# Performance work log

Measured on AMD Instinct MI355X. Metric: run time of the kernel, lower is better.

The kernel has to match this reference:

```python
import jax, jax.numpy as jnp
import numpy as np

N_NODES = 100_000
N_EDGES = 1_200_000
N_GRAPHS = 256
HIT_IN, VAR_IN = 5, 19
H = 64            # hit_embed_dim (h_feat of ResGCN)
D = 128           # transformer hidden = hit + var embed
N_GNN, N_ENC, HEADS, NCLS = 6, 6, 8, 2
EPS = 1e-7        # GENConv message eps


def _ln(x, g, b, eps=1e-5):
    m = jnp.mean(x, -1, keepdims=True)
    v = jnp.mean((x - m) ** 2, -1, keepdims=True)
    return (x - m) * jax.lax.rsqrt(v + eps) * g + b


def _forward(floats, edge_index, batch):
    (x, var_data, enc_W, enc_b, ln_g, ln_b, t_param, mlp1_W, mlp1_b,
     mlpn_g, mlpn_b, mlp2_W, mlp2_b, v1_W, v1_b, v2_W, v2_b, v3_W, v3_b,
     qkv_W, qkv_b, out_W, out_b, ln1_g, ln1_b, ff1_W, ff1_b, ff2_W, ff2_b,
     ln2_g, ln2_b, head_W, head_b) = floats
    src, dst = edge_index[0], edge_index[1]
    N = x.shape[0]
    h = x @ enc_W + enc_b                                   # [N, H]
    for i in range(N_GNN):
        # DeepGCNLayer block='res+': norm -> relu -> conv, then residual add
        z = jax.nn.relu(_ln(h, ln_g[i], ln_b[i]))
        # GENConv aggr='softmax': per-channel segment softmax over incoming edges
        msg = jax.nn.relu(z[src]) + EPS                     # [E, H]
        s = msg * t_param[i]
        m = jax.lax.stop_gradient(jax.ops.segment_max(s, dst, num_segments=N))
        m = jnp.where(jnp.isfinite(m), m, 0.0)
        e = jnp.exp(s - m[dst])
        den = jax.ops.segment_sum(e, dst, num_segments=N)
        alpha = e / jnp.maximum(den, 1e-16)[dst]
        agg = jax.ops.segment_sum(msg * alpha, dst, num_segments=N)
        # GENConv: out = mlp(agg + x_dst); MLP = Lin(H,2H)->LN->ReLU->Lin(2H,H)
        u = z + agg
        u = jax.nn.relu(_ln(u @ mlp1_W[i] + mlp1_b[i], mlpn_g[i], mlpn_b[i]))
        u = u @ mlp2_W[i] + mlp2_b[i]
        h = h + u
    pooled = jax.ops.segment_sum(h, batch, num_segments=N_GRAPHS)  # [B, H]
    # VariableEmbed MLP 19->16->32->64
    v = jax.nn.relu(var_data @ v1_W + v1_b)
    v = jax.nn.relu(v @ v2_W + v2_b)
    v = v @ v3_W + v3_b
    # reshape(-1,1,D) -> seq_len = num_graphs, batch = 1 (post-norm encoder)
    t = jnp.concatenate([pooled, v], -1)                    # [B, D]
    S = t.shape[0]
    dh = D // HEADS
    for i in range(N_ENC):
        qkv = t @ qkv_W[i] + qkv_b[i]
        q, k, vv = jnp.split(qkv, 3, axis=-1)
        q = q.reshape(S, HEADS, dh).transpose(1, 0, 2)
        k = k.reshape(S, HEADS, dh).transpose(1, 0, 2)
        vv = vv.reshape(S, HEADS, dh).transpose(1, 0, 2)
        att = jax.nn.softmax(jnp.einsum('hqd,hkd->hqk', q, k) / jnp.sqrt(jnp.float32(dh)), axis=-1)
        o = jnp.einsum('hqk,hkd->hqd', att, vv).transpose(1, 0, 2).reshape(S, D)
        o = o @ out_W[i] + out_b[i]
        t = _ln(t + o, ln1_g[i], ln1_b[i])
        f = jax.nn.gelu(t @ ff1_W[i] + ff1_b[i], approximate=False)
        f = f @ ff2_W[i] + ff2_b[i]
        t = _ln(t + f, ln2_g[i], ln2_b[i])
    return t @ head_W + head_b                              # [B, NCLS]


FLOAT_KEYS = ['x', 'var_data', 'enc_W', 'enc_b', 'ln_g', 'ln_b', 't_param',
              'mlp1_W', 'mlp1_b', 'mlpn_g', 'mlpn_b', 'mlp2_W', 'mlp2_b',
              'v1_W', 'v1_b', 'v2_W', 'v2_b', 'v3_W', 'v3_b',
              'qkv_W', 'qkv_b', 'out_W', 'out_b', 'ln1_g', 'ln1_b',
              'ff1_W', 'ff1_b', 'ff2_W', 'ff2_b', 'ln2_g', 'ln2_b',
              'head_W', 'head_b']


def setup_inputs() -> dict:
    key = jax.random.key(0)
    ks = iter(jax.random.split(key, 64))
    def nrm(shape, s=0.05):
        return jax.random.normal(next(ks), shape, jnp.float32) * s
    return {
        'x': jax.random.normal(next(ks), (N_NODES, HIT_IN), jnp.float32),
        'edge_index': jax.random.randint(next(ks), (2, N_EDGES), 0, N_NODES),
        'batch': jnp.sort(jax.random.randint(next(ks), (N_NODES,), 0, N_GRAPHS)),
        'var_data': jax.random.normal(next(ks), (N_GRAPHS, VAR_IN), jnp.float32),
        'enc_W': nrm((HIT_IN, H)), 'enc_b': jnp.zeros((H,)),
        'ln_g': jnp.ones((N_GNN, H)), 'ln_b': jnp.zeros((N_GNN, H)),
        't_param': jnp.ones((N_GNN,)),
        'mlp1_W': nrm((N_GNN, H, 2 * H)), 'mlp1_b': jnp.zeros((N_GNN, 2 * H)),
        'mlpn_g': jnp.ones((N_GNN, 2 * H)), 'mlpn_b': jnp.zeros((N_GNN, 2 * H)),
        'mlp2_W': nrm((N_GNN, 2 * H, H)), 'mlp2_b': jnp.zeros((N_GNN, H)),
        'v1_W': nrm((VAR_IN, 16)), 'v1_b': jnp.zeros((16,)),
        'v2_W': nrm((16, 32)), 'v2_b': jnp.zeros((32,)),
        'v3_W': nrm((32, 64)), 'v3_b': jnp.zeros((64,)),
        'qkv_W': nrm((N_ENC, D, 3 * D)), 'qkv_b': jnp.zeros((N_ENC, 3 * D)),
        'out_W': nrm((N_ENC, D, D)), 'out_b': jnp.zeros((N_ENC, D)),
        'ln1_g': jnp.ones((N_ENC, D)), 'ln1_b': jnp.zeros((N_ENC, D)),
        'ff1_W': nrm((N_ENC, D, D)), 'ff1_b': jnp.zeros((N_ENC, D)),
        'ff2_W': nrm((N_ENC, D, D)), 'ff2_b': jnp.zeros((N_ENC, D)),
        'ln2_g': jnp.ones((N_ENC, D)), 'ln2_b': jnp.zeros((N_ENC, D)),
        'head_W': nrm((D, NCLS)), 'head_b': jnp.zeros((NCLS,)),
    }


def reference(x, edge_index, batch, var_data, enc_W, enc_b, ln_g, ln_b, t_param,
              mlp1_W, mlp1_b, mlpn_g, mlpn_b, mlp2_W, mlp2_b,
              v1_W, v1_b, v2_W, v2_b, v3_W, v3_b,
              qkv_W, qkv_b, out_W, out_b, ln1_g, ln1_b,
              ff1_W, ff1_b, ff2_W, ff2_b, ln2_g, ln2_b, head_W, head_b):
    floats = (x, var_data, enc_W, enc_b, ln_g, ln_b, t_param, mlp1_W, mlp1_b,
              mlpn_g, mlpn_b, mlp2_W, mlp2_b, v1_W, v1_b, v2_W, v2_b, v3_W, v3_b,
              qkv_W, qkv_b, out_W, out_b, ln1_g, ln1_b, ff1_W, ff1_b, ff2_W, ff2_b,
              ln2_g, ln2_b, head_W, head_b)
    return _forward(floats, edge_index, batch)
```

## Files before the change

### kernel.cpp

```cpp
#include <hip/hip_runtime.h>
#include <hip/hip_bf16.h>
#include <math.h>

#define NODES 100000
#define EDGES 1200000
#define NG 256

typedef unsigned short u16;
typedef unsigned int   u32;
typedef __attribute__((ext_vector_type(8))) short bf16x8;
typedef __attribute__((ext_vector_type(4))) float f32x4;

__device__ __forceinline__ u16 f2bf(float f){
  u32 u = __float_as_uint(f);
  u32 r = (u + 0x7FFFu + ((u >> 16) & 1u)) >> 16;
  return (u16)r;
}
__device__ __forceinline__ float bf2f(u16 b){ return __uint_as_float(((u32)b) << 16); }
__device__ __forceinline__ float bfL(u32 v){ return __uint_as_float(v << 16); }
__device__ __forceinline__ float bfH(u32 v){ return __uint_as_float(v & 0xFFFF0000u); }

__device__ __forceinline__ float wsum64(float v){
  v += __shfl_xor(v, 32); v += __shfl_xor(v, 16); v += __shfl_xor(v, 8);
  v += __shfl_xor(v, 4);  v += __shfl_xor(v, 2);  v += __shfl_xor(v, 1);
  return v;
}
__device__ __forceinline__ float wmax64(float v){
  v = fmaxf(v, __shfl_xor(v, 32)); v = fmaxf(v, __shfl_xor(v, 16));
  v = fmaxf(v, __shfl_xor(v, 8));  v = fmaxf(v, __shfl_xor(v, 4));
  v = fmaxf(v, __shfl_xor(v, 2));  v = fmaxf(v, __shfl_xor(v, 1));
  return v;
}
__device__ __forceinline__ float bsum256(float v, float* red){
  v = wsum64(v);
  if ((threadIdx.x & 63) == 0) red[threadIdx.x >> 6] = v;
  __syncthreads();
  float r = red[0] + red[1] + red[2] + red[3];
  __syncthreads();
  return r;
}

__global__ void k_zero2(int* counts, float* pooled){
  int i = blockIdx.x*256 + threadIdx.x;
  if (i < NODES) counts[i] = 0;
  if (i < NG*64) pooled[i] = 0.f;
}

__global__ void k_wprep(const float* __restrict__ m1W, const float* __restrict__ m2W,
                        u16* __restrict__ w1t_g, u16* __restrict__ w2t_g){
  int idx = blockIdx.x*256 + threadIdx.x;
  if (idx < 49152){
    int L = idx >> 13, r = idx & 8191, j = r >> 6, k = r & 63;
    w1t_g[idx] = f2bf(m1W[(L << 13) + k*128 + j]);
  } else if (idx < 98304){
    int t = idx - 49152;
    int L = t >> 13, r = t & 8191, j = r >> 7, k = r & 127;
    w2t_g[t] = f2bf(m2W[(L << 13) + k*64 + j]);
  }
}

__global__ void k_hist(const int* __restrict__ dst, int* __restrict__ counts){
  int e = blockIdx.x*256 + threadIdx.x;
  if (e < EDGES) atomicAdd(&counts[dst[e]], 1);
}

__global__ void k_scan1(const int* __restrict__ counts, int* __restrict__ rowptr, int* __restrict__ bsums){
  __shared__ int sd[256];
  int tid = threadIdx.x;
  int base = blockIdx.x*2048 + tid*8;
  int v[8]; int s = 0;
  #pragma unroll
  for (int i = 0; i < 8; i++){
    int idx = base + i;
    int c = (idx < NODES) ? counts[idx] : 0;
    v[i] = s; s += c;
  }
  sd[tid] = s;
  __syncthreads();
  for (int off = 1; off < 256; off <<= 1){
    int t = 0;
    if (tid >= off) t = sd[tid - off];
    __syncthreads();
    if (tid >= off) sd[tid] += t;
    __syncthreads();
  }
  int excl = (tid > 0) ? sd[tid-1] : 0;
  #pragma unroll
  for (int i = 0; i < 8; i++){
    int idx = base + i;
    if (idx < NODES) rowptr[idx] = v[i] + excl;
  }
  if (tid == 255) bsums[blockIdx.x] = sd[255];
}

__global__ void k_scan2(const int* __restrict__ bsums, int* __restrict__ boffs, int nb){
  int tid = threadIdx.x;
  int acc = 0;
  for (int j = 0; j < nb; j++){
    int b = bsums[j];
    if (j < tid) acc += b;
  }
  if (tid < nb) boffs[tid] = acc;
}

__global__ void k_scan3(int* __restrict__ rowptr, int* __restrict__ cursor, const int* __restrict__ boffs){
  int i = blockIdx.x*256 + threadIdx.x;
  if (i < NODES){
    int r = rowptr[i] + boffs[i >> 11];
    rowptr[i] = r; cursor[i] = r;
  }
  if (i == 0) rowptr[NODES] = EDGES;
}

__global__ void k_scatter(const int* __restrict__ src, const int* __restrict__ dst,
                          int* __restrict__ cursor, int* __restrict__ esrc){
  int e = blockIdx.x*256 + threadIdx.x;
  if (e < EDGES){
    int d = dst[e];
    int p = atomicAdd(&cursor[d], 1);
    esrc[p] = src[e];
  }
}

__global__ __launch_bounds__(256) void k_enc(const float* __restrict__ x,
    const float* __restrict__ encW, const float* __restrict__ encb,
    const float* __restrict__ lg, const float* __restrict__ lb,
    float* __restrict__ h, u16* __restrict__ z){
  __shared__ float we[320], wb[64], sg[64], sb[64];
  int tid = threadIdx.x;
  for (int i = tid; i < 320; i += 256) we[i] = encW[i];
  if (tid < 64){ wb[tid] = encb[tid]; sg[tid] = lg[tid]; sb[tid] = lb[tid]; }
  __syncthreads();
  int n = blockIdx.x*256 + tid;
  if (n >= NODES) return;
  float xv[5];
  #pragma unroll
  for (int k = 0; k < 5; k++) xv[k] = x[n*5 + k];
  float a[64];
  #pragma unroll
  for (int c = 0; c < 64; c++){
    float t = wb[c];
    #pragma unroll
    for (int k = 0; k < 5; k++) t += xv[k]*we[k*64 + c];
    a[c] = t;
  }
  float mean = 0.f;
  #pragma unroll
  for (int c = 0; c < 64; c++) mean += a[c];
  mean *= (1.f/64.f);
  float var = 0.f;
  #pragma unroll
  for (int c = 0; c < 64; c++){ float d = a[c]-mean; var += d*d; }
  var *= (1.f/64.f);
  float rstd = rsqrtf(var + 1e-5f);
  size_t rb = (size_t)n*64;
  #pragma unroll
  for (int c = 0; c < 64; c += 4){
    *(float4*)&h[rb + c] = make_float4(a[c], a[c+1], a[c+2], a[c+3]);
    ushort4 zv;
    zv.x = f2bf(fmaxf((a[c  ]-mean)*rstd*sg[c  ]+sb[c  ], 0.f));
    zv.y = f2bf(fmaxf((a[c+1]-mean)*rstd*sg[c+1]+sb[c+1], 0.f));
    zv.z = f2bf(fmaxf((a[c+2]-mean)*rstd*sg[c+2]+sb[c+2], 0.f));
    zv.w = f2bf(fmaxf((a[c+3]-mean)*rstd*sg[c+3]+sb[c+3], 0.f));
    *(ushort4*)&z[rb + c] = zv;
  }
}

__global__ __launch_bounds__(256) void k_agg(const u32* __restrict__ z32, u32* __restrict__ uo,
    const int* __restrict__ rowptr, const int* __restrict__ esrc,
    const float* __restrict__ tparam, int li){
  int lane = threadIdx.x & 63;
  int half = lane >> 5;
  int c2 = lane & 31;
  int n = blockIdx.x*8 + (threadIdx.x >> 6)*2 + half;
  if (n >= NODES) return;
  float tp = tparam[li];
  int beg = rowptr[n], end = rowptr[n+1];
  u32 zp = z32[(size_t)n*32 + c2];
  float zn0 = bfL(zp), zn1 = bfH(zp);
  float den0 = 0.f, num0 = 0.f, den1 = 0.f, num1 = 0.f;
  int e = beg;
  for (; e + 7 < end; e += 8){
    int si[8];
    #pragma unroll
    for (int r = 0; r < 8; r++) si[r] = esrc[e + r];
    u32 vv[8];
    #pragma unroll
    for (int r = 0; r < 8; r++) vv[r] = z32[(size_t)si[r]*32 + c2];
    #pragma unroll
    for (int r = 0; r < 8; r++){
      float m0 = bfL(vv[r]) + 1e-7f, m1 = bfH(vv[r]) + 1e-7f;
      float e0 = __expf(m0*tp), e1 = __expf(m1*tp);
      den0 += e0; num0 += m0*e0;
      den1 += e1; num1 += m1*e1;
    }
  }
  for (; e + 3 < end; e += 4){
    int si[4];
    #pragma unroll
    for (int r = 0; r < 4; r++) si[r] = esrc[e + r];
    u32 vv[4];
    #pragma unroll
    for (int r = 0; r < 4; r++) vv[r] = z32[(size_t)si[r]*32 + c2];
    #pragma unroll
    for (int r = 0; r < 4; r++){
      float m0 = bfL(vv[r]) + 1e-7f, m1 = bfH(vv[r]) + 1e-7f;
      float e0 = __expf(m0*tp), e1 = __expf(m1*tp);
      den0 += e0; num0 += m0*e0;
      den1 += e1; num1 += m1*e1;
    }
  }
  for (; e < end; ++e){
    u32 v = z32[(size_t)esrc[e]*32 + c2];
    float m0 = bfL(v) + 1e-7f, m1 = bfH(v) + 1e-7f;
    float e0 = __expf(m0*tp), e1 = __expf(m1*tp);
    den0 += e0; num0 += m0*e0;
    den1 += e1; num1 += m1*e1;
  }
  float u0 = zn0 + num0 / fmaxf(den0, 1e-16f);
  float u1 = zn1 + num1 / fmaxf(den1, 1e-16f);
  uo[(size_t)n*32 + c2] = (u32)f2bf(u0) | ((u32)f2bf(u1) << 16);
}

__global__ __launch_bounds__(256) void k_mlpm(
    const u16* __restrict__ u, float* __restrict__ h, u16* __restrict__ znext,
    float* __restrict__ pooled, const int* __restrict__ batch,
    const u16* __restrict__ w1t_g, const u16* __restrict__ w2t_g,
    const float* __restrict__ B1, const float* __restrict__ G1, const float* __restrict__ Q1,
    const float* __restrict__ B2, const float* __restrict__ GN, const float* __restrict__ BN,
    int last){
  __shared__ u16 w1t[128*88];
  __shared__ u16 w2t[64*152];
  __shared__ float cb1[128], cg1[128], cq1[128];
  __shared__ float cb2[64], cgn[64], cbn[64];
  int tid = threadIdx.x;
  const uint4* w1g = (const uint4*)w1t_g;
  const uint4* w2g = (const uint4*)w2t_g;
  for (int i = tid; i < 1024; i += 256){
    { int j = i >> 3, c = i & 7;  *(uint4*)&w1t[j*88  + c*8] = w1g[i]; }
    { int j = i >> 4, c = i & 15; *(uint4*)&w2t[j*152 + c*8] = w2g[i]; }
  }
  if (tid < 128){ cb1[tid] = B1[tid]; cg1[tid] = G1[tid]; cq1[tid] = Q1[tid]; }
  if (tid < 64){
    cb2[tid] = B2[tid];
    cgn[tid] = last ? 0.f : GN[tid];
    cbn[tid] = last ? 0.f : BN[tid];
  }
  __syncthreads();

  int w = tid >> 6, l = tid & 63, l15 = l & 15, g = l >> 4;
  int nd = w*16 + l15;
  int base0 = blockIdx.x*128;
  int hi = g >> 1;
  int s0l = ((g & 1) << 5) + l15;
  int s1l = s0l + 16;
  f32x4 zero4 = {0.f, 0.f, 0.f, 0.f};
  bf16x8 bz8 = {0,0,0,0,0,0,0,0};

  bf16x8 buA[2], buB[2];
  #pragma unroll
  for (int it = 0; it < 2; it++){
    int node = base0 + it*64 + nd;
    bool ok = node < NODES;
    buA[it] = ok ? *(const bf16x8*)&u[(size_t)node*64 +      g*8] : bz8;
    buB[it] = ok ? *(const bf16x8*)&u[(size_t)node*64 + 32 + g*8] : bz8;
  }

  #pragma unroll
  for (int it = 0; it < 2; it++){
    int node = base0 + it*64 + nd;
    bool ok = node < NODES;
    f32x4 c1[8];
    #pragma unroll
    for (int mt = 0; mt < 8; mt++) c1[mt] = zero4;
    #pragma unroll
    for (int mt = 0; mt < 8; mt++){
      bf16x8 aw0 = *(const bf16x8*)&w1t[(mt*16 + l15)*88 +      g*8];
      c1[mt] = __builtin_amdgcn_mfma_f32_16x16x32_bf16(aw0, buA[it], c1[mt], 0, 0, 0);
      bf16x8 aw1 = *(const bf16x8*)&w1t[(mt*16 + l15)*88 + 32 + g*8];
      c1[mt] = __builtin_amdgcn_mfma_f32_16x16x32_bf16(aw1, buB[it], c1[mt], 0, 0, 0);
    }
    float sum = 0.f, sq = 0.f;
    #pragma unroll
    for (int mt = 0; mt < 8; mt++){
      #pragma unroll
      for (int r = 0; r < 4; r++){
        float v = c1[mt][r] + cb1[mt*16 + g*4 + r];
        c1[mt][r] = v;
        sum += v; sq += v*v;
      }
    }
    sum += __shfl_xor(sum, 16); sum += __shfl_xor(sum, 32);
    sq  += __shfl_xor(sq, 16);  sq  += __shfl_xor(sq, 32);
    float mean = sum*(1.f/128.f);
    float var  = sq*(1.f/128.f) - mean*mean;
    float rstd = rsqrtf(fmaxf(var, 0.f) + 1e-5f);
    u32 pk0[8], pk1[8];
    #pragma unroll
    for (int mt = 0; mt < 8; mt++){
      int ch = mt*16 + g*4;
      float a0 = fmaxf((c1[mt][0]-mean)*rstd*cg1[ch  ] + cq1[ch  ], 0.f);
      float a1 = fmaxf((c1[mt][1]-mean)*rstd*cg1[ch+1] + cq1[ch+1], 0.f);
      float a2 = fmaxf((c1[mt][2]-mean)*rstd*cg1[ch+2] + cq1[ch+2], 0.f);
      float a3 = fmaxf((c1[mt][3]-mean)*rstd*cg1[ch+3] + cq1[ch+3], 0.f);
      pk0[mt] = (u32)f2bf(a0) | ((u32)f2bf(a1) << 16);
      pk1[mt] = (u32)f2bf(a2) | ((u32)f2bf(a3) << 16);
    }
    f32x4 c2[4];
    #pragma unroll
    for (int mt = 0; mt < 4; mt++) c2[mt] = zero4;
    #pragma unroll
    for (int ks = 0; ks < 4; ks++){
      u32 x0 = pk0[2*ks], x1 = pk0[2*ks+1];
      u32 y0 = pk1[2*ks], y1 = pk1[2*ks+1];
      u32 a0 = (u32)__shfl((int)x0, s0l), a1 = (u32)__shfl((int)x1, s0l);
      u32 b0 = (u32)__shfl((int)y0, s0l), b1 = (u32)__shfl((int)y1, s0l);
      u32 c0 = (u32)__shfl((int)x0, s1l), c1v = (u32)__shfl((int)x1, s1l);
      u32 d0 = (u32)__shfl((int)y0, s1l), d1 = (u32)__shfl((int)y1, s1l);
      union { u32 q[4]; bf16x8 v; } bb;
      bb.q[0] = hi ? a1 : a0;
      bb.q[1] = hi ? b1 : b0;
      bb.q[2] = hi ? c1v : c0;
      bb.q[3] = hi ? d1 : d0;
      #pragma unroll
      for (int mt = 0; mt < 4; mt++){
        bf16x8 aw = *(const bf16x8*)&w2t[(mt*16 + l15)*152 + ks*32 + g*8];
        c2[mt] = __builtin_amdgcn_mfma_f32_16x16x32_bf16(aw, bb.v, c2[mt], 0, 0, 0);
      }
    }
    if (ok){
      float out[16];
      size_t hb = (size_t)node*64;
      #pragma unroll
      for (int mt = 0; mt < 4; mt++){
        int ch = mt*16 + g*4;
        float4 hv = *(const float4*)&h[hb + ch];
        out[mt*4  ] = c2[mt][0] + cb2[ch  ] + hv.x;
        out[mt*4+1] = c2[mt][1] + cb2[ch+1] + hv.y;
        out[mt*4+2] = c2[mt][2] + cb2[ch+2] + hv.z;
        out[mt*4+3] = c2[mt][3] + cb2[ch+3] + hv.w;
      }
      if (!last){
        #pragma unroll
        for (int mt = 0; mt < 4; mt++){
          int ch = mt*16 + g*4;
          *(float4*)&h[hb + ch] = make_float4(out[mt*4], out[mt*4+1], out[mt*4+2], out[mt*4+3]);
        }
        float s2 = 0.f, q2 = 0.f;
        #pragma unroll
        for (int c = 0; c < 16; c++){ s2 += out[c]; q2 += out[c]*out[c]; }
        s2 += __shfl_xor(s2, 16); s2 += __shfl_xor(s2, 32);
        q2 += __shfl_xor(q2, 16); q2 += __shfl_xor(q2, 32);
        float m2 = s2*(1.f/64.f);
        float v2 = q2*(1.f/64.f) - m2*m2;
        float rs2 = rsqrtf(fmaxf(v2, 0.f) + 1e-5f);
        #pragma unroll
        for (int mt = 0; mt < 4; mt++){
          int ch = mt*16 + g*4;
          u16 z0 = f2bf(fmaxf((out[mt*4  ]-m2)*rs2*cgn[ch  ] + cbn[ch  ], 0.f));
          u16 z1 = f2bf(fmaxf((out[mt*4+1]-m2)*rs2*cgn[ch+1] + cbn[ch+1], 0.f));
          u16 z2 = f2bf(fmaxf((out[mt*4+2]-m2)*rs2*cgn[ch+2] + cbn[ch+2], 0.f));
          u16 z3 = f2bf(fmaxf((out[mt*4+3]-m2)*rs2*cgn[ch+3] + cbn[ch+3], 0.f));
          uint2 pk; pk.x = (u32)z0 | ((u32)z1 << 16); pk.y = (u32)z2 | ((u32)z3 << 16);
          *(uint2*)&znext[hb + ch] = pk;
        }
      } else {
        int gb = batch[node];
        #pragma unroll
        for (int c = 0; c < 16; c++){
          int ch = (c >> 2)*16 + g*4 + (c & 3);
          atomicAdd(&pooled[gb*64 + ch], out[c]);
        }
      }
    }
  }
}

__global__ __launch_bounds__(128) void k_pool2(
    const float* __restrict__ pooled, const float* __restrict__ var_data,
    const float* __restrict__ v1W, const float* __restrict__ v1b,
    const float* __restrict__ v2W, const float* __restrict__ v2b,
    const float* __restrict__ v3W, const float* __restrict__ v3b,
    float* __restrict__ t, float* __restrict__ qkvout,
    const float* __restrict__ qW, const float* __restrict__ qb){
  __shared__ float vin[19], l1[16], l2[32], tr[128];
  int c = threadIdx.x, s = blockIdx.x;
  if (c < 19) vin[c] = var_data[s*19 + c];
  __syncthreads();
  if (c < 16){
    float a = v1b[c];
    for (int k = 0; k < 19; k++) a += vin[k]*v1W[k*16 + c];
    l1[c] = fmaxf(a, 0.f);
  }
  __syncthreads();
  if (c < 32){
    float a = v2b[c];
    for (int k = 0; k < 16; k++) a += l1[k]*v2W[k*32 + c];
    l2[c] = fmaxf(a, 0.f);
  }
  __syncthreads();
  float tv;
  if (c < 64) tv = pooled[s*64 + c];
  else {
    float a = v3b[c-64];
    for (int k = 0; k < 32; k++) a += l2[k]*v3W[k*64 + (c-64)];
    tv = a;
  }
  tr[c] = tv; t[s*128 + c] = tv;
  __syncthreads();
  #pragma unroll 1
  for (int r = 0; r < 3; r++){
    int col = r*128 + c;
    float a = qb[col];
    #pragma unroll 4
    for (int k = 0; k < 128; k++) a += tr[k]*qW[k*384 + col];
    qkvout[s*384 + col] = a;
  }
}

__global__ __launch_bounds__(256) void k_attrow(
    const float* __restrict__ qkv, float* __restrict__ t, float* __restrict__ qkvout,
    const float* __restrict__ outW, const float* __restrict__ outb,
    const float* __restrict__ l1g, const float* __restrict__ l1b,
    const float* __restrict__ f1W, const float* __restrict__ f1b,
    const float* __restrict__ f2W, const float* __restrict__ f2b,
    const float* __restrict__ l2g, const float* __restrict__ l2b,
    const float* __restrict__ qW, const float* __restrict__ qb,
    const float* __restrict__ hW, const float* __restrict__ hb2,
    float* __restrict__ dout, int last){
  __shared__ float kv[8448];
  __shared__ float sc[8*260];
  __shared__ float qrow[128], orow[128], strow[128], s1row[128], sfrow[128], t2row[128];
  __shared__ float red[4];
  int tid = threadIdx.x, s = blockIdx.x;
  if (tid < 128){ qrow[tid] = qkv[(size_t)s*384 + tid]; strow[tid] = t[(size_t)s*128 + tid]; }
  for (int tile = 0; tile < 4; tile++){
    __syncthreads();
    for (int i = tid; i < 8192; i += 256){
      int r = i >> 7, c = i & 127;
      kv[r*132 + c] = qkv[(size_t)(tile*64 + r)*384 + 128 + c];
    }
    __syncthreads();
    int j = tid >> 2, sub = tid & 3;
    float d0 = 0.f, d1 = 0.f;
    #pragma unroll
    for (int d = 0; d < 16; d++){
      d0 += qrow[sub*16 + d]     * kv[j*132 + sub*16 + d];
      d1 += qrow[(sub+4)*16 + d] * kv[j*132 + (sub+4)*16 + d];
    }
    sc[sub*260     + tile*64 + j] = d0*0.25f;
    sc[(sub+4)*260 + tile*64 + j] = d1*0.25f;
  }
  __syncthreads();
  {
    int wid = tid >> 6, lane = tid & 63;
    #pragma unroll
    for (int hh = 0; hh < 2; hh++){
      int hh2 = wid*2 + hh;
      float a0 = sc[hh2*260 + lane], a1 = sc[hh2*260 + 64 + lane];
      float a2 = sc[hh2*260 + 128 + lane], a3 = sc[hh2*260 + 192 + lane];
      float m = wmax64(fmaxf(fmaxf(a0,a1), fmaxf(a2,a3)));
      float e0 = __expf(a0-m), e1 = __expf(a1-m), e2 = __expf(a2-m), e3 = __expf(a3-m);
      float sum = wsum64((e0+e1)+(e2+e3));
      float inv = 1.f/sum;
      sc[hh2*260 + lane] = e0*inv; sc[hh2*260 + 64 + lane] = e1*inv;
      sc[hh2*260 + 128 + lane] = e2*inv; sc[hh2*260 + 192 + lane] = e3*inv;
    }
  }
  float o = 0.f;
  int hme = (tid & 127) >> 4;
  for (int tile = 0; tile < 4; tile++){
    __syncthreads();
    for (int i = tid; i < 8192; i += 256){
      int r = i >> 7, c = i & 127;
      kv[r*132 + c] = qkv[(size_t)(tile*64 + r)*384 + 256 + c];
    }
    __syncthreads();
    if (tid < 128){
      #pragma unroll 4
      for (int j = 0; j < 64; j++)
        o += sc[hme*260 + tile*64 + j] * kv[j*132 + tid];
    }
  }
  if (tid < 128) orow[tid] = o;
  float acc = (tid < 128) ? outb[tid] : 0.f;
  for (int kt = 0; kt < 4; kt++){
    __syncthreads();
    for (int i = tid; i < 4096; i += 256) kv[i] = outW[(size_t)kt*4096 + i];
    __syncthreads();
    if (tid < 128){
      #pragma unroll 8
      for (int kk = 0; kk < 32; kk++) acc += orow[kt*32 + kk]*kv[kk*128 + tid];
    }
  }
  if (tid < 128) acc += strow[tid];
  float mean = bsum256((tid < 128) ? acc : 0.f, red)*(1.f/128.f);
  float d0v = (tid < 128) ? (acc - mean) : 0.f;
  float var = bsum256(d0v*d0v, red)*(1.f/128.f);
  float t1 = 0.f;
  if (tid < 128){
    t1 = d0v*rsqrtf(var + 1e-5f)*l1g[tid] + l1b[tid];
    s1row[tid] = t1;
  }
  float f = (tid < 128) ? f1b[tid] : 0.f;
  for (int kt = 0; kt < 4; kt++){
    __syncthreads();
    for (int i = tid; i < 4096; i += 256) kv[i] = f1W[(size_t)kt*4096 + i];
    __syncthreads();
    if (tid < 128){
      #pragma unroll 8
      for (int kk = 0; kk < 32; kk++) f += s1row[kt*32 + kk]*kv[kk*128 + tid];
    }
  }
  if (tid < 128){
    f = 0.5f*f*(1.f + erff(f*0.70710678118654752f));
    sfrow[tid] = f;
  }
  float g = (tid < 128) ? f2b[tid] : 0.f;
  for (int kt = 0; kt < 4; kt++){
    __syncthreads();
    for (int i = tid; i < 4096; i += 256) kv[i] = f2W[(size_t)kt*4096 + i];
    __syncthreads();
    if (tid < 128){
      #pragma unroll 8
      for (int kk = 0; kk < 32; kk++) g += sfrow[kt*32 + kk]*kv[kk*128 + tid];
    }
  }
  if (tid < 128) g += t1;
  float mean2 = bsum256((tid < 128) ? g : 0.f, red)*(1.f/128.f);
  float d2v = (tid < 128) ? (g - mean2) : 0.f;
  float var2 = bsum256(d2v*d2v, red)*(1.f/128.f);
  if (tid < 128){
    float t2 = d2v*rsqrtf(var2 + 1e-5f)*l2g[tid] + l2b[tid];
    t[(size_t)s*128 + tid] = t2;
    t2row[tid] = t2;
  }
  __syncthreads();
  if (!last){
    float a0 = qb[tid];
    float a1 = (tid < 128) ? qb[256 + tid] : 0.f;
    for (int kt = 0; kt < 8; kt++){
      __syncthreads();
      for (int i = tid; i < 6144; i += 256) kv[i] = qW[(size_t)kt*6144 + i];
      __syncthreads();
      #pragma unroll 4
      for (int kk = 0; kk < 16; kk++){
        float tv = t2row[kt*16 + kk];
        a0 += tv*kv[kk*384 + tid];
        if (tid < 128) a1 += tv*kv[kk*384 + 256 + tid];
      }
    }
    qkvout[(size_t)s*384 + tid] = a0;
    if (tid < 128) qkvout[(size_t)s*384 + 256 + tid] = a1;
  } else {
    if (tid < 2){
      float a = hb2[tid];
      for (int k = 0; k < 128; k++) a += t2row[k]*hW[k*2 + tid];
      dout[s*2 + tid] = a;
    }
  }
}

extern "C" void kernel_launch(void* const* d_in, const int* in_sizes, int n_in,
                              void* d_out, int out_size, void* d_ws, size_t ws_size,
                              hipStream_t stream){
  const float* x       = (const float*)d_in[0];
  const int*   ei      = (const int*)  d_in[1];
  const int*   batch   = (const int*)  d_in[2];
  const float* var_d   = (const float*)d_in[3];
  const float* encW    = (const float*)d_in[4];
  const float* encb    = (const float*)d_in[5];
  const float* ln_g    = (const float*)d_in[6];
  const float* ln_b    = (const float*)d_in[7];
  const float* tparam  = (const float*)d_in[8];
  const float* m1W     = (const float*)d_in[9];
  const float* m1b     = (const float*)d_in[10];
  const float* mng     = (const float*)d_in[11];
  const float* mnb     = (const float*)d_in[12];
  const float* m2W     = (const float*)d_in[13];
  const float* m2b     = (const float*)d_in[14];
  const float* v1W     = (const float*)d_in[15];
  const float* v1b     = (const float*)d_in[16];
  const float* v2W     = (const float*)d_in[17];
  const float* v2b     = (const float*)d_in[18];
  const float* v3W     = (const float*)d_in[19];
  const float* v3b     = (const float*)d_in[20];
  const float* qkvW    = (const float*)d_in[21];
  const float* qkvB    = (const float*)d_in[22];
  const float* outW    = (const float*)d_in[23];
  const float* outb    = (const float*)d_in[24];
  const float* l1g     = (const float*)d_in[25];
  const float* l1b     = (const float*)d_in[26];
  const float* f1W     = (const float*)d_in[27];
  const float* f1b     = (const float*)d_in[28];
  const float* f2W     = (const float*)d_in[29];
  const float* f2b     = (const float*)d_in[30];
  const float* l2g     = (const float*)d_in[31];
  const float* l2b     = (const float*)d_in[32];
  const float* headW   = (const float*)d_in[33];
  const float* headB   = (const float*)d_in[34];
  float* dout = (float*)d_out;

  char* wsb = (char*)d_ws;
  size_t off = 0;
  auto nxt = [&](size_t bytes)->void*{
    void* p = wsb + off;
    off += (bytes + 255) & ~(size_t)255;
    return p;
  };
  float* h      = (float*)nxt((size_t)NODES*64*4);
  u16*   z      = (u16*)  nxt((size_t)NODES*64*2);
  u16*   u      = (u16*)  nxt((size_t)NODES*64*2);
  int*   rowptr = (int*)  nxt((size_t)(NODES+1)*4);
  int*   cursor = (int*)  nxt((size_t)NODES*4);
  int*   counts = (int*)  nxt((size_t)NODES*4);
  int*   bsums  = (int*)  nxt(64*4);
  int*   boffs  = (int*)  nxt(64*4);
  int*   esrc   = (int*)  nxt((size_t)EDGES*4);
  float* pooled = (float*)nxt((size_t)NG*64*4);
  float* tbuf   = (float*)nxt((size_t)NG*128*4);
  float* qkv0   = (float*)nxt((size_t)NG*384*4);
  float* qkv1   = (float*)nxt((size_t)NG*384*4);
  u16*   w1tg   = (u16*)  nxt((size_t)49152*2);
  u16*   w2tg   = (u16*)  nxt((size_t)49152*2);
  float* qkvb[2] = { qkv0, qkv1 };

  const int* srcp = ei;
  const int* dstp = ei + EDGES;

  k_zero2  <<<391, 256, 0, stream>>>(counts, pooled);
  k_wprep  <<<384, 256, 0, stream>>>(m1W, m2W, w1tg, w2tg);
  k_hist   <<<4688, 256, 0, stream>>>(dstp, counts);
  k_scan1  <<<49, 256, 0, stream>>>(counts, rowptr, bsums);
  k_scan2  <<<1, 64, 0, stream>>>(bsums, boffs, 49);
  k_scan3  <<<391, 256, 0, stream>>>(rowptr, cursor, boffs);
  k_scatter<<<4688, 256, 0, stream>>>(srcp, dstp, cursor, esrc);
  k_enc    <<<391, 256, 0, stream>>>(x, encW, encb, ln_g, ln_b, h, z);

  for (int i = 0; i < 6; i++){
    int last = (i == 5);
    k_agg <<<12500, 256, 0, stream>>>((const u32*)z, (u32*)u, rowptr, esrc, tparam, i);
    k_mlpm<<<782, 256, 0, stream>>>(u, h, z, pooled, batch,
        w1tg + i*8192, w2tg + i*8192,
        m1b + i*128, mng + i*128, mnb + i*128,
        m2b + i*64,
        ln_g + (last ? 0 : (i+1)*64), ln_b + (last ? 0 : (i+1)*64), last);
  }

  k_pool2<<<NG, 128, 0, stream>>>(pooled, var_d, v1W, v1b, v2W, v2b, v3W, v3b,
                                  tbuf, qkv0, qkvW, qkvB);

  for (int i = 0; i < 6; i++){
    int last = (i == 5);
    k_attrow<<<NG, 256, 0, stream>>>(qkvb[i & 1], tbuf, qkvb[(i + 1) & 1],
        outW + i*16384, outb + i*128, l1g + i*128, l1b + i*128,
        f1W + i*16384, f1b + i*128, f2W + i*16384, f2b + i*128,
        l2g + i*128, l2b + i*128,
        qkvW + (size_t)(last ? 0 : (i+1))*49152, qkvB + (last ? 0 : (i+1))*384,
        headW, headB, dout, last);
  }
}
```

Baseline: 1.501 ms.

## Store residual and QKV in bf16, widen agg lanes, merge init kernels

Stores the residual stream h and the transformer QKV buffers in bf16 instead of fp32, which halves their memory traffic. Changes the aggregation kernel so each lane handles four channels with uint2 loads, giving 16 lanes per node and half as many blocks. Merges the zeroing and weight-prep kernels into one launch. Accumulating the residual in bf16 across six layers adds rounding error and risks accuracy.

Result: faster. 1.444 ms (-3.8%).

```diff
diff --git a/kernel.cpp b/kernel.cpp
--- a/kernel.cpp
+++ b/kernel.cpp
@@ -19,6 +19,7 @@
 __device__ __forceinline__ float bf2f(u16 b){ return __uint_as_float(((u32)b) << 16); }
 __device__ __forceinline__ float bfL(u32 v){ return __uint_as_float(v << 16); }
 __device__ __forceinline__ float bfH(u32 v){ return __uint_as_float(v & 0xFFFF0000u); }
+__device__ __forceinline__ u32 pk2(float a, float b){ return (u32)f2bf(a) | ((u32)f2bf(b) << 16); }
 
 __device__ __forceinline__ float wsum64(float v){
   v += __shfl_xor(v, 32); v += __shfl_xor(v, 16); v += __shfl_xor(v, 8);
@@ -40,19 +41,17 @@
   return r;
 }
 
-__global__ void k_zero2(int* counts, float* pooled){
-  int i = blockIdx.x*256 + threadIdx.x;
-  if (i < NODES) counts[i] = 0;
-  if (i < NG*64) pooled[i] = 0.f;
-}
-
-__global__ void k_wprep(const float* __restrict__ m1W, const float* __restrict__ m2W,
-                        u16* __restrict__ w1t_g, u16* __restrict__ w2t_g){
+__global__ void k_init(int* counts, float* pooled,
+                       const float* __restrict__ m1W, const float* __restrict__ m2W,
+                       u16* __restrict__ w1t_g, u16* __restrict__ w2t_g){
   int idx = blockIdx.x*256 + threadIdx.x;
+  if (idx < NODES) counts[idx] = 0;
+  if (idx < NG*64) pooled[idx] = 0.f;
   if (idx < 49152){
     int L = idx >> 13, r = idx & 8191, j = r >> 6, k = r & 63;
     w1t_g[idx] = f2bf(m1W[(L << 13) + k*128 + j]);
-  } else if (idx < 98304){
+  }
+  if (idx < 98304 && idx >= 49152){
     int t = idx - 49152;
     int L = t >> 13, r = t & 8191, j = r >> 7, k = r & 127;
     w2t_g[t] = f2bf(m2W[(L << 13) + k*64 + j]);
@@ -125,7 +124,7 @@
 __global__ __launch_bounds__(256) void k_enc(const float* __restrict__ x,
     const float* __restrict__ encW, const float* __restrict__ encb,
     const float* __restrict__ lg, const float* __restrict__ lb,
-    float* __restrict__ h, u16* __restrict__ z){
+    u16* __restrict__ hbf, u16* __restrict__ z){
   __shared__ float we[320], wb[64], sg[64], sb[64];
   int tid = threadIdx.x;
   for (int i = tid; i < 320; i += 256) we[i] = encW[i];
@@ -156,13 +155,15 @@
   size_t rb = (size_t)n*64;
   #pragma unroll
   for (int c = 0; c < 64; c += 4){
-    *(float4*)&h[rb + c] = make_float4(a[c], a[c+1], a[c+2], a[c+3]);
-    ushort4 zv;
-    zv.x = f2bf(fmaxf((a[c  ]-mean)*rstd*sg[c  ]+sb[c  ], 0.f));
-    zv.y = f2bf(fmaxf((a[c+1]-mean)*rstd*sg[c+1]+sb[c+1], 0.f));
-    zv.z = f2bf(fmaxf((a[c+2]-mean)*rstd*sg[c+2]+sb[c+2], 0.f));
-    zv.w = f2bf(fmaxf((a[c+3]-mean)*rstd*sg[c+3]+sb[c+3], 0.f));
-    *(ushort4*)&z[rb + c] = zv;
+    uint2 hv;
+    hv.x = pk2(a[c], a[c+1]); hv.y = pk2(a[c+2], a[c+3]);
+    *(uint2*)&hbf[rb + c] = hv;
+    uint2 zv;
+    zv.x = pk2(fmaxf((a[c  ]-mean)*rstd*sg[c  ]+sb[c  ], 0.f),
+               fmaxf((a[c+1]-mean)*rstd*sg[c+1]+sb[c+1], 0.f));
+    zv.y = pk2(fmaxf((a[c+2]-mean)*rstd*sg[c+2]+sb[c+2], 0.f),
+               fmaxf((a[c+3]-mean)*rstd*sg[c+3]+sb[c+3], 0.f));
+    *(uint2*)&z[rb + c] = zv;
   }
 }
 
@@ -170,60 +171,71 @@
     const int* __restrict__ rowptr, const int* __restrict__ esrc,
     const float* __restrict__ tparam, int li){
   int lane = threadIdx.x & 63;
-  int half = lane >> 5;
-  int c2 = lane & 31;
-  int n = blockIdx.x*8 + (threadIdx.x >> 6)*2 + half;
+  int q  = lane >> 4;
+  int cl = lane & 15;
+  int n = blockIdx.x*16 + (threadIdx.x >> 6)*4 + q;
   if (n >= NODES) return;
   float tp = tparam[li];
   int beg = rowptr[n], end = rowptr[n+1];
-  u32 zp = z32[(size_t)n*32 + c2];
-  float zn0 = bfL(zp), zn1 = bfH(zp);
-  float den0 = 0.f, num0 = 0.f, den1 = 0.f, num1 = 0.f;
+  const uint2* zq = (const uint2*)z32;
+  uint2 zp = zq[(size_t)n*16 + cl];
+  float zn0 = bfL(zp.x), zn1 = bfH(zp.x), zn2 = bfL(zp.y), zn3 = bfH(zp.y);
+  float den0=0.f,num0=0.f,den1=0.f,num1=0.f,den2=0.f,num2=0.f,den3=0.f,num3=0.f;
   int e = beg;
   for (; e + 7 < end; e += 8){
     int si[8];
     #pragma unroll
     for (int r = 0; r < 8; r++) si[r] = esrc[e + r];
-    u32 vv[8];
-    #pragma unroll
-    for (int r = 0; r < 8; r++) vv[r] = z32[(size_t)si[r]*32 + c2];
+    uint2 vv[8];
+    #pragma unroll
+    for (int r = 0; r < 8; r++) vv[r] = zq[(size_t)si[r]*16 + cl];
     #pragma unroll
     for (int r = 0; r < 8; r++){
-      float m0 = bfL(vv[r]) + 1e-7f, m1 = bfH(vv[r]) + 1e-7f;
-      float e0 = __expf(m0*tp), e1 = __expf(m1*tp);
+      float m0 = bfL(vv[r].x) + 1e-7f, m1 = bfH(vv[r].x) + 1e-7f;
+      float m2 = bfL(vv[r].y) + 1e-7f, m3 = bfH(vv[r].y) + 1e-7f;
+      float e0 = __expf(m0*tp), e1 = __expf(m1*tp), e2 = __expf(m2*tp), e3 = __expf(m3*tp);
       den0 += e0; num0 += m0*e0;
       den1 += e1; num1 += m1*e1;
+      den2 += e2; num2 += m2*e2;
+      den3 += e3; num3 += m3*e3;
     }
   }
   for (; e + 3 < end; e += 4){
     int si[4];
     #pragma unroll
     for (int r = 0; r < 4; r++) si[r] = esrc[e + r];
-    u32 vv[4];
-    #pragma unroll
-    for (int r = 0; r < 4; r++) vv[r] = z32[(size_t)si[r]*32 + c2];
+    uint2 vv[4];
+    #pragma unroll
+    for (int r = 0; r < 4; r++) vv[r] = zq[(size_t)si[r]*16 + cl];
     #pragma unroll
     for (int r = 0; r < 4; r++){
-      float m0 = bfL(vv[r]) + 1e-7f, m1 = bfH(vv[r]) + 1e-7f;
-      float e0 = __expf(m0*tp), e1 = __expf(m1*tp);
+      float m0 = bfL(vv[r].x) + 1e-7f, m1 = bfH(vv[r].x) + 1e-7f;
+      float m2 = bfL(vv[r].y) + 1e-7f, m3 = bfH(vv[r].y) + 1e-7f;
+      float e0 = __expf(m0*tp), e1 = __expf(m1*tp), e2 = __expf(m2*tp), e3 = __expf(m3*tp);
       den0 += e0; num0 += m0*e0;
       den1 += e1; num1 += m1*e1;
+      den2 += e2; num2 += m2*e2;
+      den3 += e3; num3 += m3*e3;
     }
   }
   for (; e < end; ++e){
-    u32 v = z32[(size_t)esrc[e]*32 + c2];
-    float m0 = bfL(v) + 1e-7f, m1 = bfH(v) + 1e-7f;
-    float e0 = __expf(m0*tp), e1 = __expf(m1*tp);
+    uint2 v = zq[(size_t)esrc[e]*16 + cl];
+    float m0 = bfL(v.x) + 1e-7f, m1 = bfH(v.x) + 1e-7f;
+    float m2 = bfL(v.y) + 1e-7f, m3 = bfH(v.y) + 1e-7f;
+    float e0 = __expf(m0*tp), e1 = __expf(m1*tp), e2 = __expf(m2*tp), e3 = __expf(m3*tp);
     den0 += e0; num0 += m0*e0;
     den1 += e1; num1 += m1*e1;
-  }
-  float u0 = zn0 + num0 / fmaxf(den0, 1e-16f);
-  float u1 = zn1 + num1 / fmaxf(den1, 1e-16f);
-  uo[(size_t)n*32 + c2] = (u32)f2bf(u0) | ((u32)f2bf(u1) << 16);
+    den2 += e2; num2 += m2*e2;
+    den3 += e3; num3 += m3*e3;
+  }
+  uint2 o;
+  o.x = pk2(zn0 + num0 / fmaxf(den0, 1e-16f), zn1 + num1 / fmaxf(den1, 1e-16f));
+  o.y = pk2(zn2 + num2 / fmaxf(den2, 1e-16f), zn3 + num3 / fmaxf(den3, 1e-16f));
+  ((uint2*)uo)[(size_t)n*16 + cl] = o;
 }
 
 __global__ __launch_bounds__(256) void k_mlpm(
-    const u16* __restrict__ u, float* __restrict__ h, u16* __restrict__ znext,
+    const u16* __restrict__ u, u16* __restrict__ hbf, u16* __restrict__ znext,
     float* __restrict__ pooled, const int* __restrict__ batch,
     const u16* __restrict__ w1t_g, const u16* __restrict__ w2t_g,
     const float* __restrict__ B1, const float* __restrict__ G1, const float* __restrict__ Q1,
@@ -303,8 +315,8 @@
       float a1 = fmaxf((c1[mt][1]-mean)*rstd*cg1[ch+1] + cq1[ch+1], 0.f);
       float a2 = fmaxf((c1[mt][2]-mean)*rstd*cg1[ch+2] + cq1[ch+2], 0.f);
       float a3 = fmaxf((c1[mt][3]-mean)*rstd*cg1[ch+3] + cq1[ch+3], 0.f);
-      pk0[mt] = (u32)f2bf(a0) | ((u32)f2bf(a1) << 16);
-      pk1[mt] = (u32)f2bf(a2) | ((u32)f2bf(a3) << 16);
+      pk0[mt] = pk2(a0, a1);
+      pk1[mt] = pk2(a2, a3);
     }
     f32x4 c2[4];
     #pragma unroll
@@ -334,17 +346,20 @@
       #pragma unroll
       for (int mt = 0; mt < 4; mt++){
         int ch = mt*16 + g*4;
-        float4 hv = *(const float4*)&h[hb + ch];
-        out[mt*4  ] = c2[mt][0] + cb2[ch  ] + hv.x;
-        out[mt*4+1] = c2[mt][1] + cb2[ch+1] + hv.y;
-        out[mt*4+2] = c2[mt][2] + cb2[ch+2] + hv.z;
-        out[mt*4+3] = c2[mt][3] + cb2[ch+3] + hv.w;
+        uint2 hv = *(const uint2*)&hbf[hb + ch];
+        out[mt*4  ] = c2[mt][0] + cb2[ch  ] + bfL(hv.x);
+        out[mt*4+1] = c2[mt][1] + cb2[ch+1] + bfH(hv.x);
+        out[mt*4+2] = c2[mt][2] + cb2[ch+2] + bfL(hv.y);
+        out[mt*4+3] = c2[mt][3] + cb2[ch+3] + bfH(hv.y);
       }
       if (!last){
         #pragma unroll
         for (int mt = 0; mt < 4; mt++){
           int ch = mt*16 + g*4;
-          *(float4*)&h[hb + ch] = make_float4(out[mt*4], out[mt*4+1], out[mt*4+2], out[mt*4+3]);
+          uint2 hv;
+          hv.x = pk2(out[mt*4  ], out[mt*4+1]);
+          hv.y = pk2(out[mt*4+2], out[mt*4+3]);
+          *(uint2*)&hbf[hb + ch] = hv;
         }
         float s2 = 0.f, q2 = 0.f;
         #pragma unroll
@@ -357,11 +372,11 @@
         #pragma unroll
         for (int mt = 0; mt < 4; mt++){
           int ch = mt*16 + g*4;
-          u16 z0 = f2bf(fmaxf((out[mt*4  ]-m2)*rs2*cgn[ch  ] + cbn[ch  ], 0.f));
-          u16 z1 = f2bf(fmaxf((out[mt*4+1]-m2)*rs2*cgn[ch+1] + cbn[ch+1], 0.f));
-          u16 z2 = f2bf(fmaxf((out[mt*4+2]-m2)*rs2*cgn[ch+2] + cbn[ch+2], 0.f));
-          u16 z3 = f2bf(fmaxf((out[mt*4+3]-m2)*rs2*cgn[ch+3] + cbn[ch+3], 0.f));
-          uint2 pk; pk.x = (u32)z0 | ((u32)z1 << 16); pk.y = (u32)z2 | ((u32)z3 << 16);
+          uint2 pk;
+          pk.x = pk2(fmaxf((out[mt*4  ]-m2)*rs2*cgn[ch  ] + cbn[ch  ], 0.f),
+                     fmaxf((out[mt*4+1]-m2)*rs2*cgn[ch+1] + cbn[ch+1], 0.f));
+          pk.y = pk2(fmaxf((out[mt*4+2]-m2)*rs2*cgn[ch+2] + cbn[ch+2], 0.f),
+                     fmaxf((out[mt*4+3]-m2)*rs2*cgn[ch+3] + cbn[ch+3], 0.f));
           *(uint2*)&znext[hb + ch] = pk;
         }
       } else {
@@ -381,7 +396,7 @@
     const float* __restrict__ v1W, const float* __restrict__ v1b,
     const float* __restrict__ v2W, const float* __restrict__ v2b,
     const float* __restrict__ v3W, const float* __restrict__ v3b,
-    float* __restrict__ t, float* __restrict__ qkvout,
+    float* __restrict__ t, u16* __restrict__ qkvout,
     const float* __restrict__ qW, const float* __restrict__ qb){
   __shared__ float vin[19], l1[16], l2[32], tr[128];
   int c = threadIdx.x, s = blockIdx.x;
@@ -414,12 +429,12 @@
     float a = qb[col];
     #pragma unroll 4
     for (int k = 0; k < 128; k++) a += tr[k]*qW[k*384 + col];
-    qkvout[s*384 + col] = a;
+    qkvout[s*384 + col] = f2bf(a);
   }
 }
 
 __global__ __launch_bounds__(256) void k_attrow(
-    const float* __restrict__ qkv, float* __restrict__ t, float* __restrict__ qkvout,
+    const u16* __restrict__ qkv, float* __restrict__ t, u16* __restrict__ qkvout,
     const float* __restrict__ outW, const float* __restrict__ outb,
     const float* __restrict__ l1g, const float* __restrict__ l1b,
     const float* __restrict__ f1W, const float* __restrict__ f1b,
@@ -433,12 +448,15 @@
   __shared__ float qrow[128], orow[128], strow[128], s1row[128], sfrow[128], t2row[128];
   __shared__ float red[4];
   int tid = threadIdx.x, s = blockIdx.x;
-  if (tid < 128){ qrow[tid] = qkv[(size_t)s*384 + tid]; strow[tid] = t[(size_t)s*128 + tid]; }
+  const u32* qkv32 = (const u32*)qkv;
+  if (tid < 128){ qrow[tid] = bf2f(qkv[(size_t)s*384 + tid]); strow[tid] = t[(size_t)s*128 + tid]; }
   for (int tile = 0; tile < 4; tile++){
     __syncthreads();
-    for (int i = tid; i < 8192; i += 256){
-      int r = i >> 7, c = i & 127;
-      kv[r*132 + c] = qkv[(size_t)(tile*64 + r)*384 + 128 + c];
+    for (int i = tid; i < 4096; i += 256){
+      int r = i >> 6, c2 = i & 63;
+      u32 v = qkv32[(size_t)(tile*64 + r)*192 + 64 + c2];
+      kv[r*132 + c2*2    ] = bfL(v);
+      kv[r*132 + c2*2 + 1] = bfH(v);
     }
     __syncthreads();
     int j = tid >> 2, sub = tid & 3;
@@ -471,9 +489,11 @@
   int hme = (tid & 127) >> 4;
   for (int tile = 0; tile < 4; tile++){
     __syncthreads();
-    for (int i = tid; i < 8192; i += 256){
-      int r = i >> 7, c = i & 127;
-      kv[r*132 + c] = qkv[(size_t)(tile*64 + r)*384 + 256 + c];
+    for (int i = tid; i < 4096; i += 256){
+      int r = i >> 6, c2 = i & 63;
+      u32 v = qkv32[(size_t)(tile*64 + r)*192 + 128 + c2];
+      kv[r*132 + c2*2    ] = bfL(v);
+      kv[r*132 + c2*2 + 1] = bfH(v);
     }
     __syncthreads();
     if (tid < 128){
@@ -550,8 +570,8 @@
         if (tid < 128) a1 += tv*kv[kk*384 + 256 + tid];
       }
     }
-    qkvout[(size_t)s*384 + tid] = a0;
-    if (tid < 128) qkvout[(size_t)s*384 + 256 + tid] = a1;
+    qkvout[(size_t)s*384 + tid] = f2bf(a0);
+    if (tid < 128) qkvout[(size_t)s*384 + 256 + tid] = f2bf(a1);
   } else {
     if (tid < 2){
       float a = hb2[tid];
@@ -608,7 +628,7 @@
     off += (bytes + 255) & ~(size_t)255;
     return p;
   };
-  float* h      = (float*)nxt((size_t)NODES*64*4);
+  u16*   h      = (u16*)  nxt((size_t)NODES*64*2);
   u16*   z      = (u16*)  nxt((size_t)NODES*64*2);
   u16*   u      = (u16*)  nxt((size_t)NODES*64*2);
   int*   rowptr = (int*)  nxt((size_t)(NODES+1)*4);
@@ -619,17 +639,16 @@
   int*   esrc   = (int*)  nxt((size_t)EDGES*4);
   float* pooled = (float*)nxt((size_t)NG*64*4);
   float* tbuf   = (float*)nxt((size_t)NG*128*4);
-  float* qkv0   = (float*)nxt((size_t)NG*384*4);
-  float* qkv1   = (float*)nxt((size_t)NG*384*4);
+  u16*   qkv0   = (u16*)  nxt((size_t)NG*384*2);
+  u16*   qkv1   = (u16*)  nxt((size_t)NG*384*2);
   u16*   w1tg   = (u16*)  nxt((size_t)49152*2);
   u16*   w2tg   = (u16*)  nxt((size_t)49152*2);
-  float* qkvb[2] = { qkv0, qkv1 };
+  u16*   qkvb[2] = { qkv0, qkv1 };
 
   const int* srcp = ei;
   const int* dstp = ei + EDGES;
 
-  k_zero2  <<<391, 256, 0, stream>>>(counts, pooled);
-  k_wprep  <<<384, 256, 0, stream>>>(m1W, m2W, w1tg, w2tg);
+  k_init   <<<391, 256, 0, stream>>>(counts, pooled, m1W, m2W, w1tg, w2tg);
   k_hist   <<<4688, 256, 0, stream>>>(dstp, counts);
   k_scan1  <<<49, 256, 0, stream>>>(counts, rowptr, bsums);
   k_scan2  <<<1, 64, 0, stream>>>(bsums, boffs, 49);
@@ -639,7 +658,7 @@
 
   for (int i = 0; i < 6; i++){
     int last = (i == 5);
-    k_agg <<<12500, 256, 0, stream>>>((const u32*)z, (u32*)u, rowptr, esrc, tparam, i);
+    k_agg <<<6250, 256, 0, stream>>>((const u32*)z, (u32*)u, rowptr, esrc, tparam, i);
     k_mlpm<<<782, 256, 0, stream>>>(u, h, z, pooled, batch,
         w1tg + i*8192, w2tg + i*8192,
         m1b + i*128, mng + i*128, mnb + i*128,
```
